# Optimization experiments

Hardware: AMD Instinct MI355X
Metric: run time of the kernel (lower is better)

The kernel has to match this reference:

```python
import jax, jax.numpy as jnp
import numpy as np

N, BS, DIM, SIZE = 512, 64, 256, 8192

def setup_inputs() -> dict:
    key = jax.random.key(0)
    k1, k2 = jax.random.split(key)
    seq = jax.random.normal(k1, (N, BS, DIM), dtype=jnp.float32)
    # codebook initialized Uniform[-1, 1] as in _reset_parameters
    vocab = jax.random.uniform(k2, (SIZE, DIM), dtype=jnp.float32, minval=-1.0, maxval=1.0)
    return {"seq": seq, "vocab": vocab}

def reference(seq, vocab):
    n, bs, d = seq.shape
    x = seq.reshape(n * bs, d)                                   # [T, D]
    # squared euclidean distances; argmin identical to cdist(p=2).argmin
    x2 = jnp.sum(x * x, axis=-1, keepdims=True)                  # [T, 1]
    v2 = jnp.sum(vocab * vocab, axis=-1)                         # [K]
    d2 = x2 - 2.0 * (x @ vocab.T) + v2                           # [T, K]
    ingredients = jnp.argmin(d2, axis=1)                          # [T]
    out = jnp.take(vocab, ingredients, axis=0).reshape(n, bs, d)  # quantized seq
    return out, ingredients.reshape(n, bs)
```

## Files before the change

### kernel.cpp

```cpp
#include <hip/hip_runtime.h>

#define T_TOTAL 32768
#define D       256
#define K       8192
#define BQ      64
#define KSPLIT  4
#define KSLICE  (K / KSPLIT)
#define NSLICE  (KSPLIT * 4)
#define NCT32   (K / 32)
#define KT_STRIDE (NCT32 * 64 * 8)
#define NQB     (T_TOTAL / BQ)

typedef _Float16 half4f   __attribute__((ext_vector_type(4)));
typedef _Float16 half8f   __attribute__((ext_vector_type(8)));
typedef float    floatx16 __attribute__((ext_vector_type(16)));

#define PARTIAL_F 1048576
#define BHALVES   2097152

__device__ __forceinline__ _Float16 hi16(float x) { return (_Float16)x; }
__device__ __forceinline__ _Float16 lo16(float x, _Float16 h) { return (_Float16)(x - (float)h); }
__device__ __forceinline__ void split4(float4 v, half4f& h, half4f& l) {
    _Float16 hx = hi16(v.x), hy = hi16(v.y), hz = hi16(v.z), hw = hi16(v.w);
    h = (half4f){hx, hy, hz, hw};
    l = (half4f){lo16(v.x, hx), lo16(v.y, hy), lo16(v.z, hz), lo16(v.w, hw)};
}

__global__ void prep_kernel(const float* __restrict__ vocab,
                            _Float16* __restrict__ bhi, _Float16* __restrict__ blo,
                            float* __restrict__ hv2) {
    const int ct = blockIdx.x;
    const int t  = threadIdx.x;
    const int k4 = t & 63;
    const int w  = t >> 6;
    const float4* voc4 = (const float4*)vocab;
    const int kt = k4 >> 2;
    const int q  = k4 & 3;
    const int fl = 32 * (q >> 1);
    const int i0 = (q & 1) * 4;
    float ss[8];
    #pragma unroll
    for (int ci = 0; ci < 8; ++ci) {
        int cc = w * 8 + ci;
        float4 v = voc4[(size_t)(ct * 32 + cc) * (D / 4) + k4];
        half4f hh, ll;
        split4(v, hh, ll);
        size_t off = (((size_t)kt * NCT32 + ct) * 64 + (cc + fl)) * 8 + i0;
        *(half4f*)&bhi[off] = hh;
        *(half4f*)&blo[off] = ll;
        ss[ci] = v.x * v.x + v.y * v.y + v.z * v.z + v.w * v.w;
    }
    #pragma unroll
    for (int ci = 0; ci < 8; ++ci) {
        float s = ss[ci];
        #pragma unroll
        for (int off = 32; off; off >>= 1) s += __shfl_down(s, off, 64);
        if ((t & 63) == 0) hv2[ct * 32 + w * 8 + ci] = 0.5f * s;
    }
}

__launch_bounds__(256, 2)
__global__ void argmin_kernel(const float* __restrict__ seq,
                              const _Float16* __restrict__ bhi,
                              const _Float16* __restrict__ blo,
                              const float* __restrict__ hv2,
                              float2* __restrict__ partial) {
    __shared__ _Float16 AhL[2 * 16 * 64 * 8];
    __shared__ _Float16 AlL[2 * 16 * 64 * 8];

    const int t    = threadIdx.x;
    const int lane = t & 63;
    const int wn   = t >> 6;
    const int bi   = blockIdx.x;
    const int slice = (bi & 7) >> 1;
    const int qb    = (bi >> 3) * 2 + (bi & 1);
    const int q0   = qb * BQ;
    const int k0   = slice * KSLICE;

    const float4* seq4 = (const float4*)seq;

    #pragma unroll
    for (int i = 0; i < 16; ++i) {
        int f   = t + 256 * i;
        int row = f >> 6;
        int d4  = f & 63;
        float4 v = seq4[(size_t)(q0 + row) * (D / 4) + d4];
        half4f h, l;
        split4(v, h, l);
        int kt = d4 >> 2, qq = d4 & 3;
        int off = (((((row >> 5) * 16 + kt) * 64) + ((row & 31) + 32 * (qq >> 1))) * 8
                   + (qq & 1) * 4)
                  ^ (kt << 3);
        *(half4f*)&AhL[off] = h;
        *(half4f*)&AlL[off] = l;
    }
    __syncthreads();

    float    best[32];
    unsigned bidxp[16];
    #pragma unroll
    for (int b = 0; b < 32; ++b) best[b] = 3.4e38f;
    #pragma unroll
    for (int b = 0; b < 16; ++b) bidxp[b] = 0u;

    const _Float16* bh_l = bhi + (size_t)lane * 8;
    const _Float16* bl_l = blo + (size_t)lane * 8;

#define PF_B(BH, BL, X) do {                                                   \
        const size_t kb_ = (size_t)((X) & 15) * KT_STRIDE + cb                 \
                           + (size_t)((X) >> 4) * 4096;                        \
        BH[0] = *(const half8f*)&bh_l[kb_];                                    \
        BH[1] = *(const half8f*)&bh_l[kb_ + 512];                              \
        BL[0] = *(const half8f*)&bl_l[kb_];                                    \
        BL[1] = *(const half8f*)&bl_l[kb_ + 512];                              \
    } while (0)

#define PF_A(AH, AL, X) do {                                                   \
        const int x_ = (X) & 15;                                               \
        const int a0_ = (((x_) * 64 + lane) * 8) ^ (x_ << 3);                  \
        const int a1_ = (((16 + x_) * 64 + lane) * 8) ^ (x_ << 3);             \
        AH[0] = *(const half8f*)&AhL[a0_];  AL[0] = *(const half8f*)&AlL[a0_]; \
        AH[1] = *(const half8f*)&AhL[a1_];  AL[1] = *(const half8f*)&AlL[a1_]; \
    } while (0)

#define MFMA_BURST(AH, AL, BH, BL) do {                                                          \
        __builtin_amdgcn_s_setprio(1);                                                           \
        acc[0][0] = __builtin_amdgcn_mfma_f32_32x32x16_f16(AL[0], BH[0], acc[0][0], 0, 0, 0);    \
        acc[1][0] = __builtin_amdgcn_mfma_f32_32x32x16_f16(AL[1], BH[0], acc[1][0], 0, 0, 0);    \
        acc[0][1] = __builtin_amdgcn_mfma_f32_32x32x16_f16(AL[0], BH[1], acc[0][1], 0, 0, 0);    \
        acc[1][1] = __builtin_amdgcn_mfma_f32_32x32x16_f16(AL[1], BH[1], acc[1][1], 0, 0, 0);    \
        acc[0][0] = __builtin_amdgcn_mfma_f32_32x32x16_f16(AH[0], BL[0], acc[0][0], 0, 0, 0);    \
        acc[1][0] = __builtin_amdgcn_mfma_f32_32x32x16_f16(AH[1], BL[0], acc[1][0], 0, 0, 0);    \
        acc[0][1] = __builtin_amdgcn_mfma_f32_32x32x16_f16(AH[0], BL[1], acc[0][1], 0, 0, 0);    \
        acc[1][1] = __builtin_amdgcn_mfma_f32_32x32x16_f16(AH[1], BL[1], acc[1][1], 0, 0, 0);    \
        acc[0][0] = __builtin_amdgcn_mfma_f32_32x32x16_f16(AH[0], BH[0], acc[0][0], 0, 0, 0);    \
        acc[1][0] = __builtin_amdgcn_mfma_f32_32x32x16_f16(AH[1], BH[0], acc[1][0], 0, 0, 0);    \
        acc[0][1] = __builtin_amdgcn_mfma_f32_32x32x16_f16(AH[0], BH[1], acc[0][1], 0, 0, 0);    \
        acc[1][1] = __builtin_amdgcn_mfma_f32_32x32x16_f16(AH[1], BH[1], acc[1][1], 0, 0, 0);    \
        __builtin_amdgcn_s_setprio(0);                                                           \
    } while (0)

    half8f bh0[2], bl0[2], bh1[2], bl1[2], bh2[2], bl2[2], bh3[2], bl3[2];
    half8f ah0[2], al0[2], ah1[2], al1[2];

    size_t cb = ((size_t)(k0 >> 5) + wn * 2) * 512;

    PF_B(bh0, bl0, 0);
    PF_B(bh1, bl1, 1);
    PF_A(ah0, al0, 0);

    #pragma unroll 1
    for (int c0i = 0; c0i < KSLICE / 256; ++c0i) {
        const int c0 = k0 + c0i * 256;

        const float hvv0 = hv2[c0 + (wn * 2 + 0) * 32 + (lane & 31)];
        const float hvv1 = hv2[c0 + (wn * 2 + 1) * 32 + (lane & 31)];

        floatx16 acc[2][2];
        #pragma unroll
        for (int mi = 0; mi < 2; ++mi)
            #pragma unroll
            for (int nj = 0; nj < 2; ++nj)
                #pragma unroll
                for (int r = 0; r < 16; ++r) acc[mi][nj][r] = 0.0f;

        #pragma unroll 1
        for (int g = 0; g < 4; ++g) {
            const int kt = g * 4;
            PF_B(bh2, bl2, kt + 2);  PF_A(ah1, al1, kt + 1);
            MFMA_BURST(ah0, al0, bh0, bl0);
            PF_B(bh3, bl3, kt + 3);  PF_A(ah0, al0, kt + 2);
            MFMA_BURST(ah1, al1, bh1, bl1);
            PF_B(bh0, bl0, kt + 4);  PF_A(ah1, al1, kt + 3);
            MFMA_BURST(ah0, al0, bh2, bl2);
            PF_B(bh1, bl1, kt + 5);  PF_A(ah0, al0, kt + 4);
            MFMA_BURST(ah1, al1, bh3, bl3);
        }
        cb += 4096;

        #pragma unroll
        for (int nj = 0; nj < 2; ++nj) {
            const float hv = nj ? hvv1 : hvv0;
            const int c = c0 + (wn * 2 + nj) * 32 + (lane & 31);
            const unsigned clo = (unsigned)c;
            const unsigned chi = (unsigned)c << 16;
            #pragma unroll
            for (int mi = 0; mi < 2; ++mi)
                #pragma unroll
                for (int r = 0; r < 16; r += 2) {
                    const int b = mi * 16 + r;
                    float s0 = hv - acc[mi][nj][r];
                    float s1 = hv - acc[mi][nj][r + 1];
                    unsigned w = bidxp[b >> 1];
                    if (s0 < best[b])     { best[b] = s0;     w = (w & 0xFFFF0000u) | clo; }
                    if (s1 < best[b + 1]) { best[b + 1] = s1; w = (w & 0x0000FFFFu) | chi; }
                    bidxp[b >> 1] = w;
                }
        }
    }

    int bidx[32];
    #pragma unroll
    for (int b = 0; b < 32; ++b)
        bidx[b] = (b & 1) ? (int)(bidxp[b >> 1] >> 16) : (int)(bidxp[b >> 1] & 0xFFFFu);

    #pragma unroll
    for (int off = 1; off < 32; off <<= 1) {
        #pragma unroll
        for (int b = 0; b < 32; ++b) {
            float ob = __shfl_xor(best[b], off, 64);
            int   oi = __shfl_xor(bidx[b], off, 64);
            if (ob < best[b] || (ob == best[b] && oi < bidx[b])) {
                best[b] = ob; bidx[b] = oi;
            }
        }
    }
    if ((lane & 31) == 0) {
        const size_t sl = (size_t)(slice * 4 + wn) * T_TOTAL;
        const int rowadd = (lane >> 5) * 4;
        #pragma unroll
        for (int mi = 0; mi < 2; ++mi)
            #pragma unroll
            for (int r = 0; r < 16; ++r) {
                int qr = q0 + mi * 32 + (r & 3) + 8 * (r >> 2) + rowadd;
                partial[sl + qr] = make_float2(best[mi * 16 + r], (float)bidx[mi * 16 + r]);
            }
    }
#undef PF_B
#undef PF_A
#undef MFMA_BURST
}

__global__ void redgather_kernel(const float* __restrict__ vocab,
                                 const float2* __restrict__ partial,
                                 float* __restrict__ out) {
    int r    = blockIdx.x * 4 + (threadIdx.x >> 6);
    int lane = threadIdx.x & 63;
    float bm = 3.4e38f;
    int   bi = 0x7fffffff;
    if (lane < 16) {
        float2 p = partial[(size_t)lane * T_TOTAL + r];
        bm = p.x; bi = (int)p.y;
    }
    #pragma unroll
    for (int off = 1; off < 16; off <<= 1) {
        float ob = __shfl_xor(bm, off, 64);
        int   oi = __shfl_xor(bi, off, 64);
        if (ob < bm || (ob == bm && oi < bi)) { bm = ob; bi = oi; }
    }
    int k = __shfl(bi, 0, 64);
    const float4* src = (const float4*)(vocab + (size_t)k * D);
    float4*       dst = (float4*)(out + (size_t)r * D);
    dst[lane] = src[lane];
    if (lane == 0) out[(size_t)T_TOTAL * D + r] = (float)k;
}

__global__ void reduce_kernel(const float2* __restrict__ partial, int* __restrict__ idx) {
    int q = blockIdx.x * 256 + threadIdx.x;
    float bm = 3.4e38f;
    int   bi = 0x7fffffff;
    #pragma unroll
    for (int s = 0; s < NSLICE; ++s) {
        float2 p = partial[(size_t)s * T_TOTAL + q];
        int pi = (int)p.y;
        if (p.x < bm || (p.x == bm && pi < bi)) { bm = p.x; bi = pi; }
    }
    idx[q] = bi;
}

__global__ void gather_kernel(const float* __restrict__ vocab,
                              const int* __restrict__ idx,
                              float* __restrict__ out) {
    int r    = blockIdx.x * 4 + (threadIdx.x >> 6);
    int lane = threadIdx.x & 63;
    int k = idx[r];
    const float4* src = (const float4*)(vocab + (size_t)k * D);
    float4*       dst = (float4*)(out + (size_t)r * D);
    dst[lane] = src[lane];
    if (lane == 0) out[(size_t)T_TOTAL * D + r] = (float)k;
}

extern "C" void kernel_launch(void* const* d_in, const int* in_sizes, int n_in,
                              void* d_out, int out_size, void* d_ws, size_t ws_size,
                              hipStream_t stream) {
    const float* seq   = (const float*)d_in[0];
    const float* vocab = (const float*)d_in[1];
    float* out = (float*)d_out;

    float* hv2 = (float*)d_ws;
    _Float16* bhi = (_Float16*)(out + PARTIAL_F);
    _Float16* blo = bhi + BHALVES;

    const size_t need_ws = (size_t)(K + 2 * NSLICE * T_TOTAL) * sizeof(float) + 256;
    const bool fused = ws_size >= need_ws;

    hipLaunchKernelGGL(prep_kernel, dim3(NCT32), dim3(256), 0, stream, vocab, bhi, blo, hv2);

    if (fused) {
        float2* partial = (float2*)(hv2 + K);
        hipLaunchKernelGGL(argmin_kernel,    dim3(NQB * KSPLIT), dim3(256), 0, stream,
                           seq, bhi, blo, hv2, partial);
        hipLaunchKernelGGL(redgather_kernel, dim3(T_TOTAL / 4),  dim3(256), 0, stream,
                           vocab, partial, out);
    } else {
        float2* partial = (float2*)d_out;
        int* idx = (int*)(hv2 + K);
        hipLaunchKernelGGL(argmin_kernel, dim3(NQB * KSPLIT), dim3(256), 0, stream,
                           seq, bhi, blo, hv2, partial);
        hipLaunchKernelGGL(reduce_kernel, dim3(T_TOTAL / 256), dim3(256), 0, stream, partial, idx);
        hipLaunchKernelGGL(gather_kernel, dim3(T_TOTAL / 4),   dim3(256), 0, stream, vocab, idx, out);
    }
}
```

Measured before the change: 494.3 us.

## Double waves per block, fold hv2 into MFMA accumulator init, merge via LDS

The argmin kernel goes from 4 to 8 waves per block. Each wave now covers one 32-column tile per 256-column chunk instead of two, so accumulators drop from four to two tiles per wave. The hand-rolled register prefetch pipeline is replaced by a simple loop that loads B directly each step. The vocab is stored negated in the prep kernel so accumulators can start at 0.5*||v||^2 and the score is read straight from the accumulator, dropping the per-element subtract. Waves 4-7 fold their partial minima into waves 0-3 through LDS before writing, which keeps the partial layout unchanged; the cost is less manual latency hiding and extra LDS synchronisation.

Result: slower. 575.1 us (+16.3%).

```diff
diff --git a/kernel.cpp b/kernel.cpp
--- a/kernel.cpp
+++ b/kernel.cpp
@@ -7,8 +7,8 @@
 #define KSPLIT  4
 #define KSLICE  (K / KSPLIT)
 #define NSLICE  (KSPLIT * 4)
-#define NCT32   (K / 32)
-#define KT_STRIDE (NCT32 * 64 * 8)
+#define NCT32   256
+#define KT16    131072
 #define NQB     (T_TOTAL / BQ)
 
 typedef _Float16 half4f   __attribute__((ext_vector_type(4)));
@@ -43,12 +43,13 @@
     for (int ci = 0; ci < 8; ++ci) {
         int cc = w * 8 + ci;
         float4 v = voc4[(size_t)(ct * 32 + cc) * (D / 4) + k4];
+        ss[ci] = v.x * v.x + v.y * v.y + v.z * v.z + v.w * v.w;
+        float4 nv = make_float4(-v.x, -v.y, -v.z, -v.w);
         half4f hh, ll;
-        split4(v, hh, ll);
+        split4(nv, hh, ll);
         size_t off = (((size_t)kt * NCT32 + ct) * 64 + (cc + fl)) * 8 + i0;
         *(half4f*)&bhi[off] = hh;
         *(half4f*)&blo[off] = ll;
-        ss[ci] = v.x * v.x + v.y * v.y + v.z * v.z + v.w * v.w;
     }
     #pragma unroll
     for (int ci = 0; ci < 8; ++ci) {
@@ -59,7 +60,7 @@
     }
 }
 
-__launch_bounds__(256, 2)
+__launch_bounds__(512, 2)
 __global__ void argmin_kernel(const float* __restrict__ seq,
                               const _Float16* __restrict__ bhi,
                               const _Float16* __restrict__ blo,
@@ -80,16 +81,16 @@
     const float4* seq4 = (const float4*)seq;
 
     #pragma unroll
-    for (int i = 0; i < 16; ++i) {
-        int f   = t + 256 * i;
+    for (int i = 0; i < 8; ++i) {
+        int f   = t + 512 * i;
         int row = f >> 6;
         int d4  = f & 63;
         float4 v = seq4[(size_t)(q0 + row) * (D / 4) + d4];
         half4f h, l;
         split4(v, h, l);
-        int kt = d4 >> 2, qq = d4 & 3;
-        int off = (((((row >> 5) * 16 + kt) * 64) + ((row & 31) + 32 * (qq >> 1))) * 8
-                   + (qq & 1) * 4)
+        int kt = d4 >> 2, q = d4 & 3;
+        int off = (((((row >> 5) * 16 + kt) * 64) + ((row & 31) + 32 * (q >> 1))) * 8
+                   + (q & 1) * 4)
                   ^ (kt << 3);
         *(half4f*)&AhL[off] = h;
         *(half4f*)&AlL[off] = l;
@@ -103,85 +104,63 @@
     #pragma unroll
     for (int b = 0; b < 16; ++b) bidxp[b] = 0u;
 
-    const _Float16* bh_l = bhi + (size_t)lane * 8;
-    const _Float16* bl_l = blo + (size_t)lane * 8;
-
-#define PF_B(BH, BL, X) do {                                                   \
-        const size_t kb_ = (size_t)((X) & 15) * KT_STRIDE + cb                 \
-                           + (size_t)((X) >> 4) * 4096;                        \
-        BH[0] = *(const half8f*)&bh_l[kb_];                                    \
-        BH[1] = *(const half8f*)&bh_l[kb_ + 512];                              \
-        BL[0] = *(const half8f*)&bl_l[kb_];                                    \
-        BL[1] = *(const half8f*)&bl_l[kb_ + 512];                              \
-    } while (0)
-
-#define PF_A(AH, AL, X) do {                                                   \
-        const int x_ = (X) & 15;                                               \
-        const int a0_ = (((x_) * 64 + lane) * 8) ^ (x_ << 3);                  \
-        const int a1_ = (((16 + x_) * 64 + lane) * 8) ^ (x_ << 3);             \
-        AH[0] = *(const half8f*)&AhL[a0_];  AL[0] = *(const half8f*)&AlL[a0_]; \
-        AH[1] = *(const half8f*)&AhL[a1_];  AL[1] = *(const half8f*)&AlL[a1_]; \
-    } while (0)
-
-#define MFMA_BURST(AH, AL, BH, BL) do {                                                          \
-        __builtin_amdgcn_s_setprio(1);                                                           \
-        acc[0][0] = __builtin_amdgcn_mfma_f32_32x32x16_f16(AL[0], BH[0], acc[0][0], 0, 0, 0);    \
-        acc[1][0] = __builtin_amdgcn_mfma_f32_32x32x16_f16(AL[1], BH[0], acc[1][0], 0, 0, 0);    \
-        acc[0][1] = __builtin_amdgcn_mfma_f32_32x32x16_f16(AL[0], BH[1], acc[0][1], 0, 0, 0);    \
-        acc[1][1] = __builtin_amdgcn_mfma_f32_32x32x16_f16(AL[1], BH[1], acc[1][1], 0, 0, 0);    \
-        acc[0][0] = __builtin_amdgcn_mfma_f32_32x32x16_f16(AH[0], BL[0], acc[0][0], 0, 0, 0);    \
-        acc[1][0] = __builtin_amdgcn_mfma_f32_32x32x16_f16(AH[1], BL[0], acc[1][0], 0, 0, 0);    \
-        acc[0][1] = __builtin_amdgcn_mfma_f32_32x32x16_f16(AH[0], BL[1], acc[0][1], 0, 0, 0);    \
-        acc[1][1] = __builtin_amdgcn_mfma_f32_32x32x16_f16(AH[1], BL[1], acc[1][1], 0, 0, 0);    \
-        acc[0][0] = __builtin_amdgcn_mfma_f32_32x32x16_f16(AH[0], BH[0], acc[0][0], 0, 0, 0);    \
-        acc[1][0] = __builtin_amdgcn_mfma_f32_32x32x16_f16(AH[1], BH[0], acc[1][0], 0, 0, 0);    \
-        acc[0][1] = __builtin_amdgcn_mfma_f32_32x32x16_f16(AH[0], BH[1], acc[0][1], 0, 0, 0);    \
-        acc[1][1] = __builtin_amdgcn_mfma_f32_32x32x16_f16(AH[1], BH[1], acc[1][1], 0, 0, 0);    \
-        __builtin_amdgcn_s_setprio(0);                                                           \
-    } while (0)
-
-    half8f bh0[2], bl0[2], bh1[2], bl1[2], bh2[2], bl2[2], bh3[2], bl3[2];
-    half8f ah0[2], al0[2], ah1[2], al1[2];
-
-    size_t cb = ((size_t)(k0 >> 5) + wn * 2) * 512;
-
-    PF_B(bh0, bl0, 0);
-    PF_B(bh1, bl1, 1);
-    PF_A(ah0, al0, 0);
-
-    #pragma unroll 1
+    const int lane8  = lane << 3;
+    const int cidx   = lane & 31;
+
+    const size_t cb0 = ((size_t)(k0 >> 5) + wn) * 512;
+    const _Float16* pbh = bhi + cb0 + lane8;
+    const _Float16* pbl = blo + cb0 + lane8;
+
+    float hvn = hv2[k0 + wn * 32 + cidx];
+
     for (int c0i = 0; c0i < KSLICE / 256; ++c0i) {
         const int c0 = k0 + c0i * 256;
 
-        const float hvv0 = hv2[c0 + (wn * 2 + 0) * 32 + (lane & 31)];
-        const float hvv1 = hv2[c0 + (wn * 2 + 1) * 32 + (lane & 31)];
-
-        floatx16 acc[2][2];
-        #pragma unroll
-        for (int mi = 0; mi < 2; ++mi)
+        floatx16 acc[2];
+        #pragma unroll
+        for (int r = 0; r < 16; ++r) { acc[0][r] = hvn; acc[1][r] = hvn; }
+
+        #pragma unroll 1
+        for (int j = 0; j < 8; ++j) {
+            half8f bh0 = *(const half8f*)pbh;
+            half8f bl0 = *(const half8f*)pbl;
+            half8f bh1 = *(const half8f*)(pbh + KT16);
+            half8f bl1 = *(const half8f*)(pbl + KT16);
+            pbh += 2 * (size_t)KT16;
+            pbl += 2 * (size_t)KT16;
+            const int ak0 = ((2 * j) << 9) + (lane8 ^ ((2 * j) << 3));
+            const int ak1 = ((2 * j + 1) << 9) + (lane8 ^ ((2 * j + 1) << 3));
+            half8f al0[2], ah0[2], al1[2], ah1[2];
             #pragma unroll
-            for (int nj = 0; nj < 2; ++nj)
-                #pragma unroll
-                for (int r = 0; r < 16; ++r) acc[mi][nj][r] = 0.0f;
-
-        #pragma unroll 1
-        for (int g = 0; g < 4; ++g) {
-            const int kt = g * 4;
-            PF_B(bh2, bl2, kt + 2);  PF_A(ah1, al1, kt + 1);
-            MFMA_BURST(ah0, al0, bh0, bl0);
-            PF_B(bh3, bl3, kt + 3);  PF_A(ah0, al0, kt + 2);
-            MFMA_BURST(ah1, al1, bh1, bl1);
-            PF_B(bh0, bl0, kt + 4);  PF_A(ah1, al1, kt + 3);
-            MFMA_BURST(ah0, al0, bh2, bl2);
-            PF_B(bh1, bl1, kt + 5);  PF_A(ah0, al0, kt + 4);
-            MFMA_BURST(ah1, al1, bh3, bl3);
+            for (int mi = 0; mi < 2; ++mi) {
+                al0[mi] = *(const half8f*)&AlL[ak0 + mi * 8192];
+                ah0[mi] = *(const half8f*)&AhL[ak0 + mi * 8192];
+                al1[mi] = *(const half8f*)&AlL[ak1 + mi * 8192];
+                ah1[mi] = *(const half8f*)&AhL[ak1 + mi * 8192];
+            }
+            __builtin_amdgcn_s_setprio(1);
+            acc[0] = __builtin_amdgcn_mfma_f32_32x32x16_f16(al0[0], bh0, acc[0], 0, 0, 0);
+            acc[1] = __builtin_amdgcn_mfma_f32_32x32x16_f16(al0[1], bh0, acc[1], 0, 0, 0);
+            acc[0] = __builtin_amdgcn_mfma_f32_32x32x16_f16(al1[0], bh1, acc[0], 0, 0, 0);
+            acc[1] = __builtin_amdgcn_mfma_f32_32x32x16_f16(al1[1], bh1, acc[1], 0, 0, 0);
+            acc[0] = __builtin_amdgcn_mfma_f32_32x32x16_f16(ah0[0], bl0, acc[0], 0, 0, 0);
+            acc[1] = __builtin_amdgcn_mfma_f32_32x32x16_f16(ah0[1], bl0, acc[1], 0, 0, 0);
+            acc[0] = __builtin_amdgcn_mfma_f32_32x32x16_f16(ah1[0], bl1, acc[0], 0, 0, 0);
+            acc[1] = __builtin_amdgcn_mfma_f32_32x32x16_f16(ah1[1], bl1, acc[1], 0, 0, 0);
+            acc[0] = __builtin_amdgcn_mfma_f32_32x32x16_f16(ah0[0], bh0, acc[0], 0, 0, 0);
+            acc[1] = __builtin_amdgcn_mfma_f32_32x32x16_f16(ah0[1], bh0, acc[1], 0, 0, 0);
+            acc[0] = __builtin_amdgcn_mfma_f32_32x32x16_f16(ah1[0], bh1, acc[0], 0, 0, 0);
+            acc[1] = __builtin_amdgcn_mfma_f32_32x32x16_f16(ah1[1], bh1, acc[1], 0, 0, 0);
+            __builtin_amdgcn_s_setprio(0);
         }
-        cb += 4096;
-
-        #pragma unroll
-        for (int nj = 0; nj < 2; ++nj) {
-            const float hv = nj ? hvv1 : hvv0;
-            const int c = c0 + (wn * 2 + nj) * 32 + (lane & 31);
+        pbh += 4096 - 16 * (size_t)KT16;
+        pbl += 4096 - 16 * (size_t)KT16;
+
+        float hvn_nx = hvn;
+        if (c0i < KSLICE / 256 - 1) hvn_nx = hv2[c0 + 256 + wn * 32 + cidx];
+
+        {
+            const int c = c0 + wn * 32 + cidx;
             const unsigned clo = (unsigned)c;
             const unsigned chi = (unsigned)c << 16;
             #pragma unroll
@@ -189,14 +168,15 @@
                 #pragma unroll
                 for (int r = 0; r < 16; r += 2) {
                     const int b = mi * 16 + r;
-                    float s0 = hv - acc[mi][nj][r];
-                    float s1 = hv - acc[mi][nj][r + 1];
+                    float s0 = acc[mi][r];
+                    float s1 = acc[mi][r + 1];
                     unsigned w = bidxp[b >> 1];
                     if (s0 < best[b])     { best[b] = s0;     w = (w & 0xFFFF0000u) | clo; }
                     if (s1 < best[b + 1]) { best[b + 1] = s1; w = (w & 0x0000FFFFu) | chi; }
                     bidxp[b >> 1] = w;
                 }
         }
+        hvn = hvn_nx;
     }
 
     int bidx[32];
@@ -215,20 +195,37 @@
             }
         }
     }
-    if ((lane & 31) == 0) {
-        const size_t sl = (size_t)(slice * 4 + wn) * T_TOTAL;
-        const int rowadd = (lane >> 5) * 4;
+
+    float2* fold = (float2*)AhL;
+    const int hi4 = (lane >> 5) * 4;
+    __syncthreads();
+    if (wn >= 4 && (lane & 31) == 0) {
         #pragma unroll
         for (int mi = 0; mi < 2; ++mi)
             #pragma unroll
             for (int r = 0; r < 16; ++r) {
-                int qr = q0 + mi * 32 + (r & 3) + 8 * (r >> 2) + rowadd;
-                partial[sl + qr] = make_float2(best[mi * 16 + r], (float)bidx[mi * 16 + r]);
+                int row = mi * 32 + (r & 3) + 8 * (r >> 2) + hi4;
+                fold[(wn - 4) * 64 + row] =
+                    make_float2(best[mi * 16 + r], (float)bidx[mi * 16 + r]);
             }
     }
-#undef PF_B
-#undef PF_A
-#undef MFMA_BURST
+    __syncthreads();
+    if (wn < 4 && (lane & 31) == 0) {
+        const size_t sl = (size_t)(slice * 4 + wn) * T_TOTAL;
+        #pragma unroll
+        for (int mi = 0; mi < 2; ++mi)
+            #pragma unroll
+            for (int r = 0; r < 16; ++r) {
+                int row = mi * 32 + (r & 3) + 8 * (r >> 2) + hi4;
+                int b = mi * 16 + r;
+                float2 p = fold[wn * 64 + row];
+                int pi = (int)p.y;
+                if (p.x < best[b] || (p.x == best[b] && pi < bidx[b])) {
+                    best[b] = p.x; bidx[b] = pi;
+                }
+                partial[sl + q0 + row] = make_float2(best[b], (float)bidx[b]);
+            }
+    }
 }
 
 __global__ void redgather_kernel(const float* __restrict__ vocab,
@@ -298,14 +295,14 @@
 
     if (fused) {
         float2* partial = (float2*)(hv2 + K);
-        hipLaunchKernelGGL(argmin_kernel,    dim3(NQB * KSPLIT), dim3(256), 0, stream,
+        hipLaunchKernelGGL(argmin_kernel,    dim3(NQB * KSPLIT), dim3(512), 0, stream,
                            seq, bhi, blo, hv2, partial);
         hipLaunchKernelGGL(redgather_kernel, dim3(T_TOTAL / 4),  dim3(256), 0, stream,
                            vocab, partial, out);
     } else {
         float2* partial = (float2*)d_out;
         int* idx = (int*)(hv2 + K);
-        hipLaunchKernelGGL(argmin_kernel, dim3(NQB * KSPLIT), dim3(256), 0, stream,
+        hipLaunchKernelGGL(argmin_kernel, dim3(NQB * KSPLIT), dim3(512), 0, stream,
                            seq, bhi, blo, hv2, partial);
         hipLaunchKernelGGL(reduce_kernel, dim3(T_TOTAL / 256), dim3(256), 0, stream, partial, idx);
         hipLaunchKernelGGL(gather_kernel, dim3(T_TOTAL / 4),   dim3(256), 0, stream, vocab, idx, out);
```
